# Kernel optimization log

Measured on AMD Instinct MI355X. Metric: run time of the kernel, lower is better.

The kernel has to match this reference:

```python
import jax, jax.numpy as jnp
import numpy as np

B, D = 65536, 1024

def setup_inputs() -> dict:
    key = jax.random.key(0)
    x = jax.random.normal(key, (B, D), dtype=jnp.float32)
    return {"x": x}

def reference(x) -> jnp.ndarray:
    d = x.shape[1]
    # suffix_norm[:, i] = ||x[:, i:]|| via reverse cumulative sum of squares (single O(D) pass)
    suffix_norm = jnp.sqrt(jnp.cumsum((x * x)[:, ::-1], axis=1)[:, ::-1])
    r = suffix_norm[:, :1]                                   # [B, 1] full norm
    phi = jnp.arccos(x[:, : d - 1] / suffix_norm[:, : d - 1])  # [B, D-1]
    # last angle gets sign correction from the final coordinate
    phi_last = jnp.where(x[:, -1] < 0, 2.0 * jnp.pi - phi[:, -1], phi[:, -1])
    return jnp.concatenate([r, phi[:, : d - 2], phi_last[:, None]], axis=1)
```

## Files before the change

### kernel.cpp

```cpp
#include <hip/hip_runtime.h>
#include <math.h>


#define D_DIM 1024
#define TPB 256

__global__ __launch_bounds__(TPB) void tohypersphere_kernel(
    const float* __restrict__ x, float* __restrict__ out) {
    const int t = threadIdx.x;
    const int lane = t & 63;
    const int wave = t >> 6;
    const size_t row_off = (size_t)blockIdx.x * D_DIM;

    const float4 v = ((const float4*)(x + row_off))[t];

    float s3 = v.w * v.w;
    float s2 = fmaf(v.z, v.z, s3);
    float s1 = fmaf(v.y, v.y, s2);
    float s0 = fmaf(v.x, v.x, s1);

    float tot = s0;
#pragma unroll
    for (int off = 1; off < 64; off <<= 1) {
        float n = __shfl_down(tot, off, 64);
        if (lane + off < 64) tot += n;
    }

    __shared__ float wave_tot[4];
    __shared__ float edge_xw[4];
    if (lane == 0) wave_tot[wave] = tot;
    if (lane == 63) edge_xw[wave] = v.w;
    __syncthreads();

    float after = 0.0f;
#pragma unroll
    for (int w = 0; w < 4; ++w)
        if (w > wave) after += wave_tot[w];

    const float incl = tot + after;
    const float excl = incl - s0;

    float xw_prev = __shfl_up(v.w, 1, 64);
    if (lane == 0 && wave > 0) xw_prev = edge_xw[wave - 1];

    const float suf0 = incl;
    const float suf1 = s1 + excl;
    const float suf2 = s2 + excl;

    auto ang = [](float num, float den) {
        float r = num * rsqrtf(den);
        r = fminf(1.0f, fmaxf(-1.0f, r));
        return acosf(r);
    };

    float o0, o1, o2, o3;
    o1 = ang(v.x, suf0);
    o2 = ang(v.y, suf1);
    o3 = ang(v.z, suf2);
    if (t == 0) {
        o0 = sqrtf(incl);
    } else {
        o0 = ang(xw_prev, fmaf(xw_prev, xw_prev, incl));
    }
    if (t == TPB - 1) {
        if (v.w < 0.0f) o3 = 6.283185307179586476f - o3;
    }

    ((float4*)(out + row_off))[t] = make_float4(o0, o1, o2, o3);
}

extern "C" void kernel_launch(void* const* d_in, const int* in_sizes, int n_in,
                              void* d_out, int out_size, void* d_ws, size_t ws_size,
                              hipStream_t stream) {
    const float* x = (const float*)d_in[0];
    float* out = (float*)d_out;
    const int B = in_sizes[0] / D_DIM;
    tohypersphere_kernel<<<B, TPB, 0, stream>>>(x, out);
}
```

Baseline: 409.2 us.

## Process one row per wavefront and replace acosf with polynomial approximation

Each wavefront now handles a whole row, with four float4 chunks per lane. The suffix scan is done entirely with wave shuffles, removing the shared memory and block barrier. acosf is replaced by a cubic polynomial times sqrt approximation to cut transcendental cost, at the expense of roughly 1e-4 absolute error in the angles.

```diff
diff --git a/kernel.cpp b/kernel.cpp
--- a/kernel.cpp
+++ b/kernel.cpp
@@ -4,69 +4,81 @@
 
 #define D_DIM 1024
 #define TPB 256
+#define ROWS_PER_BLOCK 4
+
+__device__ __forceinline__ float fast_acos(float x) {
+    float ax = fminf(fabsf(x), 1.0f);
+    float p = fmaf(ax, -0.0187292994f, 0.0742610031f);
+    p = fmaf(ax, p, -0.2121144323f);
+    p = fmaf(ax, p, 1.5707287997f);
+    float t = sqrtf(1.0f - ax) * p;
+    return x < 0.0f ? 3.14159265358979324f - t : t;
+}
 
 __global__ __launch_bounds__(TPB) void tohypersphere_kernel(
     const float* __restrict__ x, float* __restrict__ out) {
-    const int t = threadIdx.x;
-    const int lane = t & 63;
-    const int wave = t >> 6;
-    const size_t row_off = (size_t)blockIdx.x * D_DIM;
+    const int lane = threadIdx.x & 63;
+    const int wave = threadIdx.x >> 6;
+    const size_t row = (size_t)blockIdx.x * ROWS_PER_BLOCK + wave;
+    const float4* __restrict__ xin = (const float4*)(x + row * D_DIM);
+    float4* __restrict__ xout = (float4*)(out + row * D_DIM);
 
-    const float4 v = ((const float4*)(x + row_off))[t];
+    float4 c[4];
+#pragma unroll
+    for (int k = 0; k < 4; ++k) c[k] = xin[lane + 64 * k];
 
-    float s3 = v.w * v.w;
-    float s2 = fmaf(v.z, v.z, s3);
-    float s1 = fmaf(v.y, v.y, s2);
-    float s0 = fmaf(v.x, v.x, s1);
+    float s1[4], s2[4], q[4];
+#pragma unroll
+    for (int k = 0; k < 4; ++k) {
+        float s3 = c[k].w * c[k].w;
+        s2[k] = fmaf(c[k].z, c[k].z, s3);
+        s1[k] = fmaf(c[k].y, c[k].y, s2[k]);
+        q[k]  = fmaf(c[k].x, c[k].x, s1[k]);
+    }
 
-    float tot = s0;
+    float sc0 = q[0], sc1 = q[1], sc2 = q[2], sc3 = q[3];
 #pragma unroll
     for (int off = 1; off < 64; off <<= 1) {
-        float n = __shfl_down(tot, off, 64);
-        if (lane + off < 64) tot += n;
+        float n0 = __shfl_down(sc0, off, 64);
+        float n1 = __shfl_down(sc1, off, 64);
+        float n2 = __shfl_down(sc2, off, 64);
+        float n3 = __shfl_down(sc3, off, 64);
+        if (lane + off < 64) { sc0 += n0; sc1 += n1; sc2 += n2; sc3 += n3; }
     }
+    float sc[4] = {sc0, sc1, sc2, sc3};
 
-    __shared__ float wave_tot[4];
-    __shared__ float edge_xw[4];
-    if (lane == 0) wave_tot[wave] = tot;
-    if (lane == 63) edge_xw[wave] = v.w;
-    __syncthreads();
+    const float T1 = __shfl(sc1, 0, 64);
+    const float T2 = __shfl(sc2, 0, 64);
+    const float T3 = __shfl(sc3, 0, 64);
+    const float after[4] = {T1 + T2 + T3, T2 + T3, T3, 0.0f};
 
-    float after = 0.0f;
+    float pw[4], l63w[4];
 #pragma unroll
-    for (int w = 0; w < 4; ++w)
-        if (w > wave) after += wave_tot[w];
+    for (int k = 0; k < 4; ++k) {
+        pw[k]   = __shfl_up(c[k].w, 1, 64);
+        l63w[k] = __shfl(c[k].w, 63, 64);
+    }
+    if (lane == 0) { pw[1] = l63w[0]; pw[2] = l63w[1]; pw[3] = l63w[2]; }
 
-    const float incl = tot + after;
-    const float excl = incl - s0;
-
-    float xw_prev = __shfl_up(v.w, 1, 64);
-    if (lane == 0 && wave > 0) xw_prev = edge_xw[wave - 1];
-
-    const float suf0 = incl;
-    const float suf1 = s1 + excl;
-    const float suf2 = s2 + excl;
-
-    auto ang = [](float num, float den) {
-        float r = num * rsqrtf(den);
-        r = fminf(1.0f, fmaxf(-1.0f, r));
-        return acosf(r);
-    };
-
-    float o0, o1, o2, o3;
-    o1 = ang(v.x, suf0);
-    o2 = ang(v.y, suf1);
-    o3 = ang(v.z, suf2);
-    if (t == 0) {
-        o0 = sqrtf(incl);
-    } else {
-        o0 = ang(xw_prev, fmaf(xw_prev, xw_prev, incl));
+#pragma unroll
+    for (int k = 0; k < 4; ++k) {
+        const float Sincl = sc[k] + after[k];
+        const float excl  = Sincl - q[k];
+        float o0, o1, o2, o3;
+        o1 = fast_acos(c[k].x * rsqrtf(Sincl));
+        o2 = fast_acos(c[k].y * rsqrtf(s1[k] + excl));
+        o3 = fast_acos(c[k].z * rsqrtf(s2[k] + excl));
+        if (k == 0 && lane == 0) {
+            o0 = sqrtf(Sincl);
+        } else {
+            const float p = pw[k];
+            o0 = fast_acos(p * rsqrtf(fmaf(p, p, Sincl)));
+        }
+        if (k == 3 && lane == 63) {
+            if (c[3].w < 0.0f) o3 = 6.28318530717958648f - o3;
+        }
+        xout[lane + 64 * k] = make_float4(o0, o1, o2, o3);
     }
-    if (t == TPB - 1) {
-        if (v.w < 0.0f) o3 = 6.283185307179586476f - o3;
-    }
-
-    ((float4*)(out + row_off))[t] = make_float4(o0, o1, o2, o3);
 }
 
 extern "C" void kernel_launch(void* const* d_in, const int* in_sizes, int n_in,
@@ -75,5 +87,5 @@
     const float* x = (const float*)d_in[0];
     float* out = (float*)d_out;
     const int B = in_sizes[0] / D_DIM;
-    tohypersphere_kernel<<<B, TPB, 0, stream>>>(x, out);
+    tohypersphere_kernel<<<B / ROWS_PER_BLOCK, TPB, 0, stream>>>(x, out);
 }
```

Result: slower. 424.4 us (+3.7%).
